# Kernel tuning notes

Measured on AMD Instinct MI355X. Metric: run time of the kernel, lower is better.

The kernel has to match this reference:

```python
import jax, jax.numpy as jnp
import numpy as np

H = 4      # SSM / attn heads (d_model/headdim = 256/64)
WIN = 4    # attention window over bands


def _ln(x, g, b):
    m = jnp.mean(x, -1, keepdims=True)
    v = jnp.mean((x - m) ** 2, -1, keepdims=True)
    return (x - m) * jax.lax.rsqrt(v + 1e-5) * g + b


def setup_inputs() -> dict:
    key = jax.random.key(0)
    ks = jax.random.split(key, 24)
    def rn(i, shape, s=0.05):
        return jax.random.normal(ks[i], shape, jnp.float32) * s
    B, T, K, D = 2, 256, 8, 256
    return {
        "z": rn(0, (B, T, K, D), 1.0),
        "ln1_g": jnp.ones((D,), jnp.float32), "ln1_b": jnp.zeros((D,), jnp.float32),
        "Wx": rn(1, (D, D)), "conv_w": rn(2, (D, 4), 0.3), "Wz": rn(3, (D, D)),
        "Wb": rn(4, (D, H * 128)), "Wc": rn(5, (D, H * 128)), "Wdt": rn(6, (D, H)),
        "dt_bias": rn(7, (H,), 0.5), "A_log": rn(8, (H,), 0.5), "theta": rn(9, (H,), 1.0),
        "D_skip": rn(10, (H,), 1.0), "mimo_U": rn(11, (H, H), 0.5), "mimo_V": rn(12, (H, H), 0.5),
        "Wout": rn(13, (D, D)),
        "ln2_g": jnp.ones((D,), jnp.float32), "ln2_b": jnp.zeros((D,), jnp.float32),
        "attn_in_w": rn(14, (3 * D, D)), "attn_in_b": rn(15, (3 * D,), 0.02),
        "attn_out_w": rn(16, (D, D)), "attn_out_b": jnp.zeros((D,), jnp.float32),
        "ln3_g": jnp.ones((D,), jnp.float32), "ln3_b": jnp.zeros((D,), jnp.float32),
        "Wg": rn(17, (D, 4 * D)), "Wu": rn(18, (D, 4 * D)), "Wd": rn(19, (4 * D, D)),
    }


def _forward(z, ln1_g, ln1_b, Wx, conv_w, Wz, Wb, Wc, Wdt, dt_bias, A_log, theta,
             D_skip, mimo_U, mimo_V, Wout, ln2_g, ln2_b, attn_in_w, attn_in_b,
             attn_out_w, attn_out_b, ln3_g, ln3_b, Wg, Wu, Wd):
    B, T, K, D = z.shape
    P = D // H
    N = Wb.shape[1] // H
    # ---------- (a) intra-band Mamba3 (complex MIMO selective scan) ----------
    u = _ln(z, ln1_g, ln1_b)
    u = jnp.transpose(u, (0, 2, 1, 3)).reshape(B * K, T, D)   # [BK,T,D]
    x = u @ Wx
    # causal depthwise conv1d, kernel 4
    xp = jnp.pad(x, ((0, 0), (3, 0), (0, 0)))
    x = sum(xp[:, k:k + T, :] * conv_w[:, k] for k in range(4))
    x = jax.nn.silu(x)
    xh = x.reshape(B * K, T, H, P)
    Bm = (u @ Wb).reshape(B * K, T, H, N)
    Cm = (u @ Wc).reshape(B * K, T, H, N)
    Mmix = mimo_U @ mimo_V.T                                  # rank-r cross-head coupling
    Bm = jnp.einsum('hg,btgn->bthn', Mmix, Bm)
    dt = jax.nn.softplus(u @ Wdt + dt_bias)                   # [BK,T,H]
    A = -jnp.exp(A_log)                                       # stable real decay
    mag = jnp.exp(dt * A)
    ph = dt * theta                                           # harmonic rotation
    ar, ai = mag * jnp.cos(ph), mag * jnp.sin(ph)
    xs = tuple(jnp.moveaxis(t, 1, 0) for t in (xh, Bm, Cm, dt, ar, ai))
    h0 = jnp.zeros((B * K, H, N, P), x.dtype)

    def step(carry, s):
        h_re, h_im = carry
        xt, bt, ct, dtt, art, ait = s
        dBx = (dtt[:, :, None, None] * bt[:, :, :, None]) * xt[:, :, None, :]
        nr = art[:, :, None, None] * h_re - ait[:, :, None, None] * h_im + dBx
        ni = art[:, :, None, None] * h_im + ait[:, :, None, None] * h_re
        return (nr, ni), jnp.einsum('bhn,bhnp->bhp', ct, nr)   # Re(C . h)

    _, ys = jax.lax.scan(step, (h0, h0), xs)                  # ys: [T,BK,H,P]
    y = jnp.moveaxis(ys, 0, 1) + D_skip[None, None, :, None] * xh
    y = y.reshape(B * K, T, D) * jax.nn.silu(u @ Wz)
    y = y @ Wout
    z = z + jnp.transpose(y.reshape(B, K, T, D), (0, 2, 1, 3))
    # ---------- (b) inter-band windowed attention ----------
    zn = _ln(z, ln2_g, ln2_b).reshape(B * T, K, D)
    qkv = zn @ attn_in_w.T + attn_in_b
    q, k_, v = jnp.split(qkv, 3, axis=-1)
    hd = D // H
    def hs(t):
        return t.reshape(B * T, K // WIN, WIN, H, hd).transpose(0, 1, 3, 2, 4)
    q, k_, v = hs(q), hs(k_), hs(v)
    s = jnp.einsum('mwhqd,mwhkd->mwhqk', q, k_) * jnp.float32(1.0 / np.sqrt(hd))
    a = jax.nn.softmax(s, axis=-1)
    o = jnp.einsum('mwhqk,mwhkd->mwhqd', a, v).transpose(0, 1, 3, 2, 4).reshape(B * T, K, D)
    z = z + (o @ attn_out_w.T + attn_out_b).reshape(B, T, K, D)
    # ---------- (c) SwiGLU FFN ----------
    zf = _ln(z, ln3_g, ln3_b)
    z = z + (jax.nn.silu(zf @ Wg) * (zf @ Wu)) @ Wd
    return z


def reference(z, ln1_g, ln1_b, Wx, conv_w, Wz, Wb, Wc, Wdt, dt_bias, A_log, theta,
              D_skip, mimo_U, mimo_V, Wout, ln2_g, ln2_b, attn_in_w, attn_in_b,
              attn_out_w, attn_out_b, ln3_g, ln3_b, Wg, Wu, Wd):
    return _forward(z, ln1_g, ln1_b, Wx, conv_w, Wz, Wb, Wc, Wdt, dt_bias, A_log,
                    theta, D_skip, mimo_U, mimo_V, Wout, ln2_g, ln2_b, attn_in_w,
                    attn_in_b, attn_out_w, attn_out_b, ln3_g, ln3_b, Wg, Wu, Wd)
```

## Files before the change

### kernel.cpp

```cpp
#include <hip/hip_runtime.h>
#include <hip/hip_bf16.h>
#include <math.h>

typedef __hip_bfloat16 bf16;
typedef __attribute__((ext_vector_type(8))) short s16x8;
typedef __attribute__((ext_vector_type(4))) float f32x4;

__device__ __forceinline__ float siluf(float x) { return x / (1.f + __expf(-x)); }
__device__ __forceinline__ float bits2f(unsigned short u) {
    union { float f; unsigned i; } v; v.i = ((unsigned)u) << 16; return v.f;
}
__device__ __forceinline__ unsigned short f2bits(float f) {
    return (unsigned short)__bfloat16_as_ushort(__float2bfloat16(f));
}

#define KFL 1024
#define OFF_UB   (768*KFL)
#define OFF_DTV  (1280*KFL)
#define OFF_BMB  (1344*KFL)
#define OFF_CMB  (2368*KFL)
#define OFF_ZGB  (3392*KFL)
#define OFF_XB   (3904*KFL)
#define OFF_X2T  (4928*KFL)
#define OFF_P    (5440*KFL)
#define OFF_YGB  (7488*KFL)
#define OFF_Z2   (8000*KFL)
#define OFF_ZFB  (9024*KFL)
#define OFF_GG   OFF_BMB

#define W_BCZX 0
#define W_OUT  393216
#define W_QKV  458752
#define W_AO   655360
#define W_GU   720896
#define W_D    1245184

__global__ __launch_bounds__(256) void prep_ln1_kernel(
    const float* __restrict__ Wx, const float* __restrict__ Wb,
    const float* __restrict__ Wc, const float* __restrict__ Wz,
    const float* __restrict__ Wo, const float* __restrict__ Wqkv,
    const float* __restrict__ Wao, const float* __restrict__ Wg,
    const float* __restrict__ Wu, const float* __restrict__ Wd,
    const float* __restrict__ U, const float* __restrict__ V,
    unsigned short* __restrict__ wout,
    const float* __restrict__ z, const float* __restrict__ g1,
    const float* __restrict__ b1, const float* __restrict__ Wdt,
    const float* __restrict__ dt_bias,
    unsigned short* __restrict__ u, float4* __restrict__ dtv4)
{
    __shared__ __align__(16) float smem[64 * 65];
    int blk = blockIdx.x;
    int tid = threadIdx.x;
    if (blk < 368) {
        if (blk >= 304) {
            int off = blk - 304;
            const float* src; int dst, base;
            if (off < 48) { src = Wqkv; dst = W_QKV; base = off * 4096; }
            else          { src = Wao;  dst = W_AO;  base = (off - 48) * 4096; }
            #pragma unroll
            for (int i = 0; i < 16; i++) {
                int idx = base + tid + i * 256;
                wout[dst + idx] = f2bits(src[idx]);
            }
            return;
        }
        float* lds = smem;
        const float* src; int srcN, n0, sc0, k0, dstoff, dstK, mix = 0, t;
        if (blk < 32)       { t = blk;       src = Wb; srcN = 512;  dstoff = W_BCZX; dstK = 256;
                              n0 = (t >> 2) * 64;        sc0 = 0; k0 = (t & 3) * 64; mix = 1; }
        else if (blk < 64)  { t = blk - 32;  src = Wc; srcN = 512;  dstoff = W_BCZX; dstK = 256;
                              n0 = 512 + (t >> 2) * 64;  sc0 = (t >> 2) * 64; k0 = (t & 3) * 64; }
        else if (blk < 80)  { t = blk - 64;  src = Wz; srcN = 256;  dstoff = W_BCZX; dstK = 256;
                              n0 = 1024 + (t >> 2) * 64; sc0 = (t >> 2) * 64; k0 = (t & 3) * 64; }
        else if (blk < 96)  { t = blk - 80;  src = Wx; srcN = 256;  dstoff = W_BCZX; dstK = 256;
                              n0 = 1280 + (t >> 2) * 64; sc0 = (t >> 2) * 64; k0 = (t & 3) * 64; }
        else if (blk < 112) { t = blk - 96;  src = Wo; srcN = 256;  dstoff = W_OUT;  dstK = 256;
                              n0 = (t >> 2) * 64;        sc0 = n0; k0 = (t & 3) * 64; }
        else if (blk < 176) { t = blk - 112; src = Wg; srcN = 1024; dstoff = W_GU;   dstK = 256;
                              n0 = (t >> 2) * 64;        sc0 = n0; k0 = (t & 3) * 64; }
        else if (blk < 240) { t = blk - 176; src = Wu; srcN = 1024; dstoff = W_GU;   dstK = 256;
                              n0 = 1024 + (t >> 2) * 64; sc0 = (t >> 2) * 64; k0 = (t & 3) * 64; }
        else                { t = blk - 240; src = Wd; srcN = 256;  dstoff = W_D;    dstK = 1024;
                              n0 = (t >> 4) * 64;        sc0 = n0; k0 = (t & 15) * 64; }
        if (mix) {
            int h = n0 >> 7, scol = n0 & 127;
            float mm[4];
            #pragma unroll
            for (int g = 0; g < 4; g++) {
                float s = 0.f;
                #pragma unroll
                for (int j = 0; j < 4; j++) s += U[h * 4 + j] * V[g * 4 + j];
                mm[g] = s;
            }
            #pragma unroll
            for (int i = 0; i < 16; i++) {
                int idx = tid + i * 256;
                int kk = idx >> 6, nn = idx & 63;
                const float* row = src + (size_t)(k0 + kk) * 512 + scol + nn;
                lds[kk * 65 + nn] = mm[0] * row[0] + mm[1] * row[128]
                                  + mm[2] * row[256] + mm[3] * row[384];
            }
        } else {
            #pragma unroll
            for (int i = 0; i < 16; i++) {
                int idx = tid + i * 256;
                int kk = idx >> 6, nn = idx & 63;
                lds[kk * 65 + nn] = src[(size_t)(k0 + kk) * srcN + sc0 + nn];
            }
        }
        __syncthreads();
        #pragma unroll
        for (int i = 0; i < 16; i++) {
            int idx = tid + i * 256;
            int nn = idx >> 6, kk = idx & 63;
            wout[dstoff + (size_t)(n0 + nn) * dstK + k0 + kk] = f2bits(lds[kk * 65 + nn]);
        }
        return;
    }
    int r = blk - 368;
    float* lds = smem;
    float* dts = smem + 4;
    int t = r & 255, bk = r >> 8;
    int b_ = bk >> 3, k = bk & 7;
    int srcr = ((b_ * 256 + t) * 8 + k) * 256;
    int d = tid;
    float x = z[srcr + d];
    float v = x;
    #pragma unroll
    for (int off = 32; off; off >>= 1) v += __shfl_xor(v, off, 64);
    if ((d & 63) == 0) lds[d >> 6] = v;
    __syncthreads();
    float mean = (lds[0] + lds[1] + lds[2] + lds[3]) * (1.f / 256.f);
    __syncthreads();
    float c = x - mean;
    v = c * c;
    #pragma unroll
    for (int off = 32; off; off >>= 1) v += __shfl_xor(v, off, 64);
    if ((d & 63) == 0) lds[d >> 6] = v;
    __syncthreads();
    float var = (lds[0] + lds[1] + lds[2] + lds[3]) * (1.f / 256.f);
    float uval = c * rsqrtf(var + 1e-5f) * g1[d] + b1[d];
    u[r * 256 + d] = f2bits(uval);
    float4 wv = *(const float4*)(Wdt + d * 4);
    float q0 = uval * wv.x, q1 = uval * wv.y, q2 = uval * wv.z, q3 = uval * wv.w;
    #pragma unroll
    for (int off = 32; off; off >>= 1) {
        q0 += __shfl_xor(q0, off, 64);
        q1 += __shfl_xor(q1, off, 64);
        q2 += __shfl_xor(q2, off, 64);
        q3 += __shfl_xor(q3, off, 64);
    }
    if ((d & 63) == 0) {
        int w = d >> 6;
        dts[w * 4 + 0] = q0; dts[w * 4 + 1] = q1;
        dts[w * 4 + 2] = q2; dts[w * 4 + 3] = q3;
    }
    __syncthreads();
    if (d == 0) {
        float dv[4];
        #pragma unroll
        for (int h = 0; h < 4; h++) {
            float xx = dts[h] + dts[4 + h] + dts[8 + h] + dts[12 + h] + dt_bias[h];
            dv[h] = (xx > 20.f) ? xx : log1pf(__expf(xx));
        }
        dtv4[r] = make_float4(dv[0], dv[1], dv[2], dv[3]);
    }
}

__global__ __launch_bounds__(256) void gemm_bczx(
    const unsigned short* __restrict__ A, const unsigned short* __restrict__ Bt,
    unsigned short* __restrict__ bmb, unsigned short* __restrict__ cmb,
    unsigned short* __restrict__ zgb, unsigned short* __restrict__ xb)
{
    __shared__ __align__(16) unsigned short As[64 * 72];
    __shared__ __align__(16) unsigned short Bs[128 * 72];
    const int K = 256;
    int tid = threadIdx.x;
    int n0 = blockIdx.x * 128, m0 = blockIdx.y * 64;
    int w = tid >> 6, l = tid & 63;
    int mwave = (w >> 1) * 32, nwave = (w & 1) * 64;
    f32x4 acc[2][4] = {};
    int srow = tid >> 3, sc = (tid & 7) * 8;
    const unsigned short* Ap = A + (size_t)(m0 + srow) * K + sc;
    const unsigned short* Bp = Bt + (size_t)(n0 + srow) * K + sc;
    int lq = l & 15, lh = l >> 4;
    uint4 a0 = *(const uint4*)(Ap);
    uint4 a1 = *(const uint4*)(Ap + (size_t)32 * K);
    uint4 b0 = *(const uint4*)(Bp);
    uint4 b1 = *(const uint4*)(Bp + (size_t)32 * K);
    uint4 b2 = *(const uint4*)(Bp + (size_t)64 * K);
    uint4 b3 = *(const uint4*)(Bp + (size_t)96 * K);
    for (int k0 = 0; k0 < K; k0 += 64) {
        if (k0) __syncthreads();
        *(uint4*)&As[srow * 72 + sc] = a0;
        *(uint4*)&As[(srow + 32) * 72 + sc] = a1;
        *(uint4*)&Bs[srow * 72 + sc] = b0;
        *(uint4*)&Bs[(srow + 32) * 72 + sc] = b1;
        *(uint4*)&Bs[(srow + 64) * 72 + sc] = b2;
        *(uint4*)&Bs[(srow + 96) * 72 + sc] = b3;
        __syncthreads();
        if (k0 + 64 < K) {
            a0 = *(const uint4*)(Ap + k0 + 64);
            a1 = *(const uint4*)(Ap + (size_t)32 * K + k0 + 64);
            b0 = *(const uint4*)(Bp + k0 + 64);
            b1 = *(const uint4*)(Bp + (size_t)32 * K + k0 + 64);
            b2 = *(const uint4*)(Bp + (size_t)64 * K + k0 + 64);
            b3 = *(const uint4*)(Bp + (size_t)96 * K + k0 + 64);
        }
        #pragma unroll
        for (int kk = 0; kk < 2; kk++) {
            int kof = kk * 32 + lh * 8;
            s16x8 bfr[4];
            #pragma unroll
            for (int nf = 0; nf < 4; nf++)
                bfr[nf] = *(const s16x8*)&Bs[(nwave + nf * 16 + lq) * 72 + kof];
            #pragma unroll
            for (int mf = 0; mf < 2; mf++) {
                s16x8 af = *(const s16x8*)&As[(mwave + mf * 16 + lq) * 72 + kof];
                #pragma unroll
                for (int nf = 0; nf < 4; nf++)
                    acc[mf][nf] = __builtin_amdgcn_mfma_f32_16x16x32_bf16(af, bfr[nf], acc[mf][nf], 0, 0, 0);
            }
        }
    }
    #pragma unroll
    for (int mf = 0; mf < 2; mf++) {
        #pragma unroll
        for (int nf = 0; nf < 4; nf++) {
            int n = n0 + nwave + nf * 16 + lq;
            #pragma unroll
            for (int r = 0; r < 4; r++) {
                int m = m0 + mwave + mf * 16 + lh * 4 + r;
                float v = acc[mf][nf][r];
                if (n < 512)       bmb[(size_t)m * 512 + n] = f2bits(v);
                else if (n < 1024) cmb[(size_t)m * 512 + (n - 512)] = f2bits(v);
                else if (n < 1280) zgb[(size_t)m * 256 + (n - 1024)] = f2bits(siluf(v));
                else               xb[(size_t)m * 256 + (n - 1280)] = f2bits(v);
            }
        }
    }
}

__global__ __launch_bounds__(256) void s_conv_kernel(
    const unsigned short* __restrict__ cmb, const unsigned short* __restrict__ bmb,
    const float4* __restrict__ dtv4, const float* __restrict__ A_log,
    const float* __restrict__ theta, unsigned short* __restrict__ P,
    const unsigned short* __restrict__ xb, const float* __restrict__ cw,
    unsigned short* __restrict__ x2t)
{
    __shared__ __align__(16) char smem[39936];
    int blk = blockIdx.x;
    int tid = threadIdx.x;
    if (blk >= 192) {
        int c = blk - 192;
        int bhid = c >> 2, tt = c & 3;
        int bk = bhid >> 2, h = bhid & 3;
        int t0 = tt * 64;
        float* tile = (float*)smem;
        #pragma unroll
        for (int i = 0; i < 17; i++) {
            int idx = tid + i * 256;
            if (idx < 67 * 64) {
                int tr = idx >> 6, dd = idx & 63;
                int t = t0 - 3 + tr;
                tile[tr * 65 + dd] = (t >= 0)
                    ? bits2f(xb[(size_t)(bk * 256 + t) * 256 + h * 64 + dd]) : 0.f;
            }
        }
        __syncthreads();
        int wv_ = tid >> 6, lt = tid & 63;
        #pragma unroll 4
        for (int pi = 0; pi < 16; pi++) {
            int p = wv_ * 16 + pi;
            float4 wv = *(const float4*)(cw + (h * 64 + p) * 4);
            float acc = tile[lt * 65 + p] * wv.x + tile[(lt + 1) * 65 + p] * wv.y +
                        tile[(lt + 2) * 65 + p] * wv.z + tile[(lt + 3) * 65 + p] * wv.w;
            x2t[(size_t)(bhid * 64 + p) * 256 + t0 + lt] = f2bits(siluf(acc));
        }
        return;
    }
    int map = blk >> 6;
    int bh = blk & 63;
    int bx = (map == 2) ? 1 : 0;
    int by = (map == 0) ? 0 : 1;
    int bk = bh >> 2, h = bh & 3;
    unsigned short* As = (unsigned short*)smem;
    unsigned short* Bs = As + 128 * 72;
    float* mAs = (float*)(smem + 36864);
    float* phs = mAs + 256;
    float* dss = phs + 256;
    int srow = tid >> 3, sc = (tid & 7) * 8;
    const unsigned short* Ap = cmb + (size_t)(bk * 256 + by * 128 + srow) * 512 + h * 128 + sc;
    const unsigned short* Bp = bmb + (size_t)(bk * 256 + bx * 128 + srow) * 512 + h * 128 + sc;
    uint4 a0 = *(const uint4*)(Ap);
    uint4 a1 = *(const uint4*)(Ap + (size_t)32 * 512);
    uint4 a2 = *(const uint4*)(Ap + (size_t)64 * 512);
    uint4 a3 = *(const uint4*)(Ap + (size_t)96 * 512);
    uint4 b0 = *(const uint4*)(Bp);
    uint4 b1 = *(const uint4*)(Bp + (size_t)32 * 512);
    uint4 b2 = *(const uint4*)(Bp + (size_t)64 * 512);
    uint4 b3 = *(const uint4*)(Bp + (size_t)96 * 512);
    {
        float4 dv = dtv4[bk * 256 + tid];
        float dth = (h == 0) ? dv.x : (h == 1) ? dv.y : (h == 2) ? dv.z : dv.w;
        float Ah = -__expf(A_log[h]);
        float th = theta[h];
        float a = dth * Ah, p = dth * th;
        dss[tid] = dth;
        int lane = tid & 63, wv = tid >> 6;
        #pragma unroll
        for (int off = 1; off < 64; off <<= 1) {
            float ta = __shfl_up(a, off, 64);
            float tp = __shfl_up(p, off, 64);
            if (lane >= off) { a += ta; p += tp; }
        }
        if (lane == 63) { mAs[wv] = a; phs[wv] = p; }
        __syncthreads();
        float offA = 0.f, offP = 0.f;
        #pragma unroll
        for (int j = 0; j < 3; j++)
            if (j < wv) { offA += mAs[j]; offP += phs[j]; }
        __syncthreads();
        mAs[tid] = a + offA;
        phs[tid] = p + offP;
        __syncthreads();
    }
    int w = tid >> 6, l = tid & 63;
    int mwave = (w >> 1) * 64, nwave = (w & 1) * 64;
    int lq = l & 15, lh = l >> 4;
    unsigned short* Pout = P + (size_t)bh * 65536;
    f32x4 acc[4][4] = {};
    for (int k0 = 0; k0 < 128; k0 += 64) {
        __syncthreads();
        *(uint4*)&As[srow * 72 + sc] = a0;
        *(uint4*)&As[(srow + 32) * 72 + sc] = a1;
        *(uint4*)&As[(srow + 64) * 72 + sc] = a2;
        *(uint4*)&As[(srow + 96) * 72 + sc] = a3;
        *(uint4*)&Bs[srow * 72 + sc] = b0;
        *(uint4*)&Bs[(srow + 32) * 72 + sc] = b1;
        *(uint4*)&Bs[(srow + 64) * 72 + sc] = b2;
        *(uint4*)&Bs[(srow + 96) * 72 + sc] = b3;
        __syncthreads();
        if (k0 + 64 < 128) {
            a0 = *(const uint4*)(Ap + k0 + 64);
            a1 = *(const uint4*)(Ap + (size_t)32 * 512 + k0 + 64);
            a2 = *(const uint4*)(Ap + (size_t)64 * 512 + k0 + 64);
            a3 = *(const uint4*)(Ap + (size_t)96 * 512 + k0 + 64);
            b0 = *(const uint4*)(Bp + k0 + 64);
            b1 = *(const uint4*)(Bp + (size_t)32 * 512 + k0 + 64);
            b2 = *(const uint4*)(Bp + (size_t)64 * 512 + k0 + 64);
            b3 = *(const uint4*)(Bp + (size_t)96 * 512 + k0 + 64);
        }
        #pragma unroll
        for (int kk = 0; kk < 2; kk++) {
            int kof = kk * 32 + lh * 8;
            s16x8 bfr[4];
            #pragma unroll
            for (int nf = 0; nf < 4; nf++)
                bfr[nf] = *(const s16x8*)&Bs[(nwave + nf * 16 + lq) * 72 + kof];
            #pragma unroll
            for (int mf = 0; mf < 4; mf++) {
                s16x8 af = *(const s16x8*)&As[(mwave + mf * 16 + lq) * 72 + kof];
                #pragma unroll
                for (int nf = 0; nf < 4; nf++)
                    acc[mf][nf] = __builtin_amdgcn_mfma_f32_16x16x32_bf16(af, bfr[nf], acc[mf][nf], 0, 0, 0);
            }
        }
    }
    #pragma unroll
    for (int mf = 0; mf < 4; mf++) {
        float tmv[4], tpv[4]; int tg[4];
        #pragma unroll
        for (int r = 0; r < 4; r++) {
            tg[r] = by * 128 + mwave + mf * 16 + lh * 4 + r;
            tmv[r] = mAs[tg[r]];
            tpv[r] = phs[tg[r]];
        }
        #pragma unroll
        for (int nf = 0; nf < 4; nf++) {
            int s = bx * 128 + nwave + nf * 16 + lq;
            float ms = mAs[s];
            float ps = phs[s];
            float ds = dss[s];
            #pragma unroll
            for (int r = 0; r < 4; r++) {
                float wgt = (s <= tg[r])
                    ? __expf(tmv[r] - ms) * __cosf(tpv[r] - ps) * ds : 0.f;
                Pout[tg[r] * 256 + s] = f2bits(acc[mf][nf][r] * wgt);
            }
        }
    }
}

__global__ __launch_bounds__(256) void gemm_y(
    const unsigned short* __restrict__ P, const unsigned short* __restrict__ x2t,
    const unsigned short* __restrict__ zgb, const float* __restrict__ Dsk,
    unsigned short* __restrict__ ygb)
{
    int by = blockIdx.x, bh = blockIdx.y;
    int bk = bh >> 2, h = bh & 3;
    int t0 = by * 32;
    int tid = threadIdx.x;
    int w = tid >> 6, l = tid & 63;
    int mw = (w >> 1) * 16, nw = (w & 1) * 32;
    int lq = l & 15, lh = l >> 4;
    __shared__ __align__(16) unsigned short As[32 * 72];
    __shared__ __align__(16) unsigned short Bs[64 * 72];
    f32x4 acc[2] = {};
    int srow = tid >> 3, sc = (tid & 7) * 8;
    const unsigned short* Ap = P + (size_t)bh * 65536 + (size_t)(t0 + srow) * 256 + sc;
    const unsigned short* Bp = x2t + (size_t)bh * 16384 + (size_t)srow * 256 + sc;
    int kmax = ((by >> 1) + 1) * 64;
    uint4 a0 = *(const uint4*)(Ap);
    uint4 b0 = *(const uint4*)(Bp);
    uint4 b1 = *(const uint4*)(Bp + (size_t)32 * 256);
    for (int k0 = 0; k0 < kmax; k0 += 64) {
        if (k0) __syncthreads();
        *(uint4*)&As[(srow & 31) * 72 + sc] = a0;
        *(uint4*)&Bs[srow * 72 + sc] = b0;
        *(uint4*)&Bs[(srow + 32) * 72 + sc] = b1;
        __syncthreads();
        if (k0 + 64 < kmax) {
            a0 = *(const uint4*)(Ap + k0 + 64);
            b0 = *(const uint4*)(Bp + k0 + 64);
            b1 = *(const uint4*)(Bp + (size_t)32 * 256 + k0 + 64);
        }
        #pragma unroll
        for (int kk = 0; kk < 2; kk++) {
            int kof = kk * 32 + lh * 8;
            s16x8 af = *(const s16x8*)&As[(mw + lq) * 72 + kof];
            #pragma unroll
            for (int nf = 0; nf < 2; nf++) {
                s16x8 bf = *(const s16x8*)&Bs[(nw + nf * 16 + lq) * 72 + kof];
                acc[nf] = __builtin_amdgcn_mfma_f32_16x16x32_bf16(af, bf, acc[nf], 0, 0, 0);
            }
        }
    }
    float dsk = Dsk[h];
    #pragma unroll
    for (int nf = 0; nf < 2; nf++) {
        int p = nw + nf * 16 + lq;
        #pragma unroll
        for (int r = 0; r < 4; r++) {
            int t = t0 + mw + lh * 4 + r;
            float xv = bits2f(x2t[(size_t)bh * 16384 + p * 256 + t]);
            float zg = bits2f(zgb[(size_t)(bk * 256 + t) * 256 + h * 64 + p]);
            ygb[(size_t)(bk * 256 + t) * 256 + h * 64 + p] =
                f2bits((acc[nf][r] + dsk * xv) * zg);
        }
    }
}

__global__ __launch_bounds__(512) void mid_kernel(
    const unsigned short* __restrict__ ygb, const unsigned short* __restrict__ wts,
    const float* __restrict__ zin,
    const float* __restrict__ g2, const float* __restrict__ b2,
    const float* __restrict__ qbias, const float* __restrict__ obias,
    const float* __restrict__ g3, const float* __restrict__ b3,
    float* __restrict__ z2, unsigned short* __restrict__ zfb)
{
    __shared__ __align__(16) char smem[65024];
    unsigned short* Bs = (unsigned short*)smem;
    unsigned short* As = (unsigned short*)(smem + 36864);
    unsigned short* zn = (unsigned short*)(smem + 39168);
    float* z1s = (float*)(smem + 47616);
    float (*partS)[8] = (float(*)[8])(smem + 64000);
    float (*partQ)[8] = (float(*)[8])(smem + 64512);
    unsigned short* qk = (unsigned short*)smem;

    const int K = 256;
    int tid = threadIdx.x;
    int m0 = blockIdx.x * 16;
    int w = tid >> 6, l = tid & 63;
    int nw = w * 32;
    int lq = l & 15, lh = l >> 4;
    int srow = tid >> 3, sc = (tid & 7) * 8;

    {
        int rb = m0 + (srow & 15);
        int irow = ((rb >> 11) * 8 + (rb & 7)) * 256 + ((rb >> 3) & 255);
        const unsigned short* Ap = ygb + (size_t)irow * K + sc;
        const unsigned short* Bp = wts + W_OUT + (size_t)srow * K + sc;
        f32x4 acc[2] = {};
        uint4 a0 = *(const uint4*)(Ap);
        uint4 c0 = *(const uint4*)(Bp);
        uint4 c1 = *(const uint4*)(Bp + (size_t)64 * K);
        uint4 c2 = *(const uint4*)(Bp + (size_t)128 * K);
        uint4 c3 = *(const uint4*)(Bp + (size_t)192 * K);
        for (int k0 = 0; k0 < K; k0 += 64) {
            if (k0) __syncthreads();
            if (tid < 128) *(uint4*)&As[srow * 72 + sc] = a0;
            *(uint4*)&Bs[srow * 72 + sc] = c0;
            *(uint4*)&Bs[(srow + 64) * 72 + sc] = c1;
            *(uint4*)&Bs[(srow + 128) * 72 + sc] = c2;
            *(uint4*)&Bs[(srow + 192) * 72 + sc] = c3;
            __syncthreads();
            if (k0 + 64 < K) {
                a0 = *(const uint4*)(Ap + k0 + 64);
                c0 = *(const uint4*)(Bp + k0 + 64);
                c1 = *(const uint4*)(Bp + (size_t)64 * K + k0 + 64);
                c2 = *(const uint4*)(Bp + (size_t)128 * K + k0 + 64);
                c3 = *(const uint4*)(Bp + (size_t)192 * K + k0 + 64);
            }
            #pragma unroll
            for (int kk = 0; kk < 2; kk++) {
                int kof = kk * 32 + lh * 8;
                s16x8 af = *(const s16x8*)&As[lq * 72 + kof];
                #pragma unroll
                for (int nf = 0; nf < 2; nf++) {
                    s16x8 bf = *(const s16x8*)&Bs[(nw + nf * 16 + lq) * 72 + kof];
                    acc[nf] = __builtin_amdgcn_mfma_f32_16x16x32_bf16(af, bf, acc[nf], 0, 0, 0);
                }
            }
        }
        #pragma unroll
        for (int r = 0; r < 4; r++) {
            int row = lh * 4 + r;
            float s = 0.f, q = 0.f;
            #pragma unroll
            for (int nf = 0; nf < 2; nf++) {
                float v = acc[nf][r] + zin[(size_t)(m0 + row) * 256 + nw + nf * 16 + lq];
                acc[nf][r] = v;
                s += v; q += v * v;
            }
            #pragma unroll
            for (int off = 1; off < 16; off <<= 1) {
                s += __shfl_xor(s, off, 64);
                q += __shfl_xor(q, off, 64);
            }
            if (lq == 0) { partS[row][w] = s; partQ[row][w] = q; }
        }
        __syncthreads();
        float gv[2], bbv[2];
        #pragma unroll
        for (int nf = 0; nf < 2; nf++) {
            gv[nf] = g2[nw + nf * 16 + lq];
            bbv[nf] = b2[nw + nf * 16 + lq];
        }
        #pragma unroll
        for (int r = 0; r < 4; r++) {
            int row = lh * 4 + r;
            float sum = 0.f, sq = 0.f;
            #pragma unroll
            for (int j = 0; j < 8; j++) { sum += partS[row][j]; sq += partQ[row][j]; }
            float mean = sum * (1.f / 256.f);
            float var = sq * (1.f / 256.f) - mean * mean;
            float rstd = rsqrtf(var + 1e-5f);
            #pragma unroll
            for (int nf = 0; nf < 2; nf++) {
                int n = nw + nf * 16 + lq;
                float v = acc[nf][r];
                z1s[row * 256 + n] = v;
                zn[row * 264 + n] = f2bits((v - mean) * rstd * gv[nf] + bbv[nf]);
            }
        }
    }

    f32x4 aq0[2] = {}, aq1[2] = {}, aq2[2] = {};
#define QKV_PASS(PIDX, AQ) do { \
    const unsigned short* Bp2 = wts + W_QKV + (size_t)((PIDX) * 256 + srow) * 256 + sc; \
    uint4 d0 = *(const uint4*)(Bp2); \
    uint4 d1 = *(const uint4*)(Bp2 + (size_t)64 * 256); \
    uint4 d2 = *(const uint4*)(Bp2 + (size_t)128 * 256); \
    uint4 d3 = *(const uint4*)(Bp2 + (size_t)192 * 256); \
    for (int k0 = 0; k0 < 256; k0 += 64) { \
        __syncthreads(); \
        *(uint4*)&Bs[srow * 72 + sc] = d0; \
        *(uint4*)&Bs[(srow + 64) * 72 + sc] = d1; \
        *(uint4*)&Bs[(srow + 128) * 72 + sc] = d2; \
        *(uint4*)&Bs[(srow + 192) * 72 + sc] = d3; \
        __syncthreads(); \
        if (k0 + 64 < 256) { \
            d0 = *(const uint4*)(Bp2 + k0 + 64); \
            d1 = *(const uint4*)(Bp2 + (size_t)64 * 256 + k0 + 64); \
            d2 = *(const uint4*)(Bp2 + (size_t)128 * 256 + k0 + 64); \
            d3 = *(const uint4*)(Bp2 + (size_t)192 * 256 + k0 + 64); \
        } \
        _Pragma("unroll") \
        for (int kk = 0; kk < 2; kk++) { \
            int kof = kk * 32 + lh * 8; \
            s16x8 af = *(const s16x8*)&zn[lq * 264 + k0 + kof]; \
            _Pragma("unroll") \
            for (int nf = 0; nf < 2; nf++) { \
                s16x8 bf = *(const s16x8*)&Bs[(nw + nf * 16 + lq) * 72 + kof]; \
                AQ[nf] = __builtin_amdgcn_mfma_f32_16x16x32_bf16(af, bf, AQ[nf], 0, 0, 0); \
            } \
        } \
    } \
} while (0)
    QKV_PASS(0, aq0);
    QKV_PASS(1, aq1);
    QKV_PASS(2, aq2);
#undef QKV_PASS

    __syncthreads();
#define QKV_STORE(PIDX, AQ) do { \
    _Pragma("unroll") \
    for (int nf = 0; nf < 2; nf++) { \
        int n = (PIDX) * 256 + nw + nf * 16 + lq; \
        float bb = qbias[n]; \
        _Pragma("unroll") \
        for (int r = 0; r < 4; r++) \
            qk[(lh * 4 + r) * 776 + n] = f2bits(AQ[nf][r] + bb); \
    } \
} while (0)
    QKV_STORE(0, aq0);
    QKV_STORE(1, aq1);
    QKV_STORE(2, aq2);
#undef QKV_STORE
    __syncthreads();
    {
        int hh = w & 3;
        int half = w >> 2;
        int d = l;
        #pragma unroll
        for (int wi = 0; wi < 2; wi++) {
            int w4 = half * 2 + wi;
            int r0 = w4 * 4;
            float qv[4], kv[4], vv[4];
            #pragma unroll
            for (int j = 0; j < 4; j++) {
                qv[j] = bits2f(qk[(r0 + j) * 776 + hh * 64 + d]);
                kv[j] = bits2f(qk[(r0 + j) * 776 + 256 + hh * 64 + d]);
                vv[j] = bits2f(qk[(r0 + j) * 776 + 512 + hh * 64 + d]);
            }
            float sc_[4][4];
            #pragma unroll
            for (int qi = 0; qi < 4; qi++)
                #pragma unroll
                for (int ki = 0; ki < 4; ki++) {
                    float v = qv[qi] * kv[ki];
                    #pragma unroll
                    for (int off = 32; off; off >>= 1) v += __shfl_xor(v, off, 64);
                    sc_[qi][ki] = v * 0.125f;
                }
            #pragma unroll
            for (int qi = 0; qi < 4; qi++) {
                float mx = fmaxf(fmaxf(sc_[qi][0], sc_[qi][1]), fmaxf(sc_[qi][2], sc_[qi][3]));
                float e0 = __expf(sc_[qi][0] - mx), e1 = __expf(sc_[qi][1] - mx);
                float e2 = __expf(sc_[qi][2] - mx), e3 = __expf(sc_[qi][3] - mx);
                float inv = 1.f / (e0 + e1 + e2 + e3);
                float ov = (e0 * vv[0] + e1 * vv[1] + e2 * vv[2] + e3 * vv[3]) * inv;
                zn[(r0 + qi) * 264 + hh * 64 + d] = f2bits(ov);
            }
        }
    }

    {
        f32x4 ac4[2] = {};
        const unsigned short* Bp4 = wts + W_AO + (size_t)srow * K + sc;
        uint4 c0 = *(const uint4*)(Bp4);
        uint4 c1 = *(const uint4*)(Bp4 + (size_t)64 * K);
        uint4 c2 = *(const uint4*)(Bp4 + (size_t)128 * K);
        uint4 c3 = *(const uint4*)(Bp4 + (size_t)192 * K);
        for (int k0 = 0; k0 < K; k0 += 64) {
            __syncthreads();
            *(uint4*)&Bs[srow * 72 + sc] = c0;
            *(uint4*)&Bs[(srow + 64) * 72 + sc] = c1;
            *(uint4*)&Bs[(srow + 128) * 72 + sc] = c2;
            *(uint4*)&Bs[(srow + 192) * 72 + sc] = c3;
            __syncthreads();
            if (k0 + 64 < K) {
                c0 = *(const uint4*)(Bp4 + k0 + 64);
                c1 = *(const uint4*)(Bp4 + (size_t)64 * K + k0 + 64);
                c2 = *(const uint4*)(Bp4 + (size_t)128 * K + k0 + 64);
                c3 = *(const uint4*)(Bp4 + (size_t)192 * K + k0 + 64);
            }
            #pragma unroll
            for (int kk = 0; kk < 2; kk++) {
                int kof = kk * 32 + lh * 8;
                s16x8 af = *(const s16x8*)&zn[lq * 264 + k0 + kof];
                #pragma unroll
                for (int nf = 0; nf < 2; nf++) {
                    s16x8 bf = *(const s16x8*)&Bs[(nw + nf * 16 + lq) * 72 + kof];
                    ac4[nf] = __builtin_amdgcn_mfma_f32_16x16x32_bf16(af, bf, ac4[nf], 0, 0, 0);
                }
            }
        }
        float bv[2], gv[2], bbv[2];
        #pragma unroll
        for (int nf = 0; nf < 2; nf++) {
            int n = nw + nf * 16 + lq;
            bv[nf] = obias[n];
            gv[nf] = g3[n];
            bbv[nf] = b3[n];
        }
        #pragma unroll
        for (int r = 0; r < 4; r++) {
            int row = lh * 4 + r;
            float s = 0.f, q = 0.f;
            #pragma unroll
            for (int nf = 0; nf < 2; nf++) {
                float v = ac4[nf][r] + bv[nf] + z1s[row * 256 + nw + nf * 16 + lq];
                ac4[nf][r] = v;
                s += v; q += v * v;
            }
            #pragma unroll
            for (int off = 1; off < 16; off <<= 1) {
                s += __shfl_xor(s, off, 64);
                q += __shfl_xor(q, off, 64);
            }
            if (lq == 0) { partS[row][w] = s; partQ[row][w] = q; }
        }
        __syncthreads();
        #pragma unroll
        for (int r = 0; r < 4; r++) {
            int row = lh * 4 + r;
            float sum = 0.f, sq = 0.f;
            #pragma unroll
            for (int j = 0; j < 8; j++) { sum += partS[row][j]; sq += partQ[row][j]; }
            float mean = sum * (1.f / 256.f);
            float var = sq * (1.f / 256.f) - mean * mean;
            float rstd = rsqrtf(var + 1e-5f);
            size_t ro = (size_t)(m0 + row) * 256;
            #pragma unroll
            for (int nf = 0; nf < 2; nf++) {
                int n = nw + nf * 16 + lq;
                float v = ac4[nf][r];
                z2[ro + n] = v;
                zfb[ro + n] = f2bits((v - mean) * rstd * gv[nf] + bbv[nf]);
            }
        }
    }
}

__global__ __launch_bounds__(256) void gemm_gu2(
    const unsigned short* __restrict__ A, const unsigned short* __restrict__ Wgu,
    unsigned short* __restrict__ gg)
{
    const int K = 256;
    __shared__ __align__(16) unsigned short As[64 * 72];
    __shared__ __align__(16) unsigned short Bgs[64 * 72];
    __shared__ __align__(16) unsigned short Bus[64 * 72];
    int tid = threadIdx.x;
    int n0 = blockIdx.x * 64, m0 = blockIdx.y * 64;
    int w = tid >> 6, l = tid & 63;
    int mwave = (w >> 1) * 32, nwave = (w & 1) * 32;
    int lq = l & 15, lh = l >> 4;
    f32x4 ag[2][2] = {}, au[2][2] = {};
    int srow = tid >> 3, sc = (tid & 7) * 8;
    const unsigned short* Ap = A + (size_t)(m0 + srow) * K + sc;
    const unsigned short* Bgp = Wgu + (size_t)(n0 + srow) * K + sc;
    const unsigned short* Bup = Wgu + (size_t)(1024 + n0 + srow) * K + sc;
    uint4 a0 = *(const uint4*)(Ap);
    uint4 a1 = *(const uint4*)(Ap + (size_t)32 * K);
    uint4 bg0 = *(const uint4*)(Bgp);
    uint4 bg1 = *(const uint4*)(Bgp + (size_t)32 * K);
    uint4 bu0 = *(const uint4*)(Bup);
    uint4 bu1 = *(const uint4*)(Bup + (size_t)32 * K);
    for (int k0 = 0; k0 < K; k0 += 64) {
        if (k0) __syncthreads();
        *(uint4*)&As[srow * 72 + sc] = a0;
        *(uint4*)&As[(srow + 32) * 72 + sc] = a1;
        *(uint4*)&Bgs[srow * 72 + sc] = bg0;
        *(uint4*)&Bgs[(srow + 32) * 72 + sc] = bg1;
        *(uint4*)&Bus[srow * 72 + sc] = bu0;
        *(uint4*)&Bus[(srow + 32) * 72 + sc] = bu1;
        __syncthreads();
        if (k0 + 64 < K) {
            a0 = *(const uint4*)(Ap + k0 + 64);
            a1 = *(const uint4*)(Ap + (size_t)32 * K + k0 + 64);
            bg0 = *(const uint4*)(Bgp + k0 + 64);
            bg1 = *(const uint4*)(Bgp + (size_t)32 * K + k0 + 64);
            bu0 = *(const uint4*)(Bup + k0 + 64);
            bu1 = *(const uint4*)(Bup + (size_t)32 * K + k0 + 64);
        }
        #pragma unroll
        for (int kk = 0; kk < 2; kk++) {
            int kof = kk * 32 + lh * 8;
            s16x8 bgr[2], bur[2];
            #pragma unroll
            for (int nf = 0; nf < 2; nf++) {
                bgr[nf] = *(const s16x8*)&Bgs[(nwave + nf * 16 + lq) * 72 + kof];
                bur[nf] = *(const s16x8*)&Bus[(nwave + nf * 16 + lq) * 72 + kof];
            }
            #pragma unroll
            for (int mf = 0; mf < 2; mf++) {
                s16x8 af = *(const s16x8*)&As[(mwave + mf * 16 + lq) * 72 + kof];
                #pragma unroll
                for (int nf = 0; nf < 2; nf++) {
                    ag[mf][nf] = __builtin_amdgcn_mfma_f32_16x16x32_bf16(af, bgr[nf], ag[mf][nf], 0, 0, 0);
                    au[mf][nf] = __builtin_amdgcn_mfma_f32_16x16x32_bf16(af, bur[nf], au[mf][nf], 0, 0, 0);
                }
            }
        }
    }
    #pragma unroll
    for (int mf = 0; mf < 2; mf++) {
        #pragma unroll
        for (int nf = 0; nf < 2; nf++) {
            int n = n0 + nwave + nf * 16 + lq;
            #pragma unroll
            for (int r = 0; r < 4; r++) {
                int m = m0 + mwave + mf * 16 + lh * 4 + r;
                gg[(size_t)m * 1024 + n] = f2bits(siluf(ag[mf][nf][r]) * au[mf][nf][r]);
            }
        }
    }
}

__global__ __launch_bounds__(256) void gemm_d2(
    const unsigned short* __restrict__ gg, const unsigned short* __restrict__ Bt,
    const float* __restrict__ resid, float* __restrict__ out)
{
    __shared__ __align__(16) unsigned short As[64 * 72];
    __shared__ __align__(16) unsigned short Bs[32 * 72];
    const int K = 1024, N = 256;
    int tid = threadIdx.x;
    int n0 = blockIdx.x * 32, m0 = blockIdx.y * 64;
    int w = tid >> 6, l = tid & 63;
    int mw = (w >> 1) * 32, nw = (w & 1) * 16;
    f32x4 acc[2] = {};
    int srow = tid >> 3, sc = (tid & 7) * 8;
    const unsigned short* Ap = gg + (size_t)(m0 + srow) * K + sc;
    const unsigned short* Bp = Bt + (size_t)(n0 + (srow & 31)) * K + sc;
    int lq = l & 15, lh = l >> 4;
    uint4 a0 = *(const uint4*)(Ap);
    uint4 a1 = *(const uint4*)(Ap + (size_t)32 * K);
    uint4 b0 = *(const uint4*)(Bp);
    for (int k0 = 0; k0 < K; k0 += 64) {
        if (k0) __syncthreads();
        *(uint4*)&As[srow * 72 + sc] = a0;
        *(uint4*)&As[(srow + 32) * 72 + sc] = a1;
        *(uint4*)&Bs[(srow & 31) * 72 + sc] = b0;
        __syncthreads();
        if (k0 + 64 < K) {
            a0 = *(const uint4*)(Ap + k0 + 64);
            a1 = *(const uint4*)(Ap + (size_t)32 * K + k0 + 64);
            b0 = *(const uint4*)(Bp + k0 + 64);
        }
        #pragma unroll
        for (int kk = 0; kk < 2; kk++) {
            int kof = kk * 32 + lh * 8;
            s16x8 bf = *(const s16x8*)&Bs[(nw + lq) * 72 + kof];
            #pragma unroll
            for (int mf = 0; mf < 2; mf++) {
                s16x8 af = *(const s16x8*)&As[(mw + mf * 16 + lq) * 72 + kof];
                acc[mf] = __builtin_amdgcn_mfma_f32_16x16x32_bf16(af, bf, acc[mf], 0, 0, 0);
            }
        }
    }
    int n = n0 + nw + lq;
    #pragma unroll
    for (int mf = 0; mf < 2; mf++) {
        #pragma unroll
        for (int r = 0; r < 4; r++) {
            int m = m0 + mw + mf * 16 + lh * 4 + r;
            out[(size_t)m * N + n] = acc[mf][r] + resid[(size_t)m * N + n];
        }
    }
}

extern "C" void kernel_launch(void* const* d_in, const int* in_sizes, int n_in,
                              void* d_out, int out_size, void* d_ws, size_t ws_size,
                              hipStream_t stream)
{
    const float* z         = (const float*)d_in[0];
    const float* ln1_g     = (const float*)d_in[1];
    const float* ln1_b     = (const float*)d_in[2];
    const float* Wx        = (const float*)d_in[3];
    const float* conv_w    = (const float*)d_in[4];
    const float* Wz        = (const float*)d_in[5];
    const float* Wb        = (const float*)d_in[6];
    const float* Wc        = (const float*)d_in[7];
    const float* Wdt       = (const float*)d_in[8];
    const float* dt_bias   = (const float*)d_in[9];
    const float* A_log     = (const float*)d_in[10];
    const float* theta     = (const float*)d_in[11];
    const float* D_skip    = (const float*)d_in[12];
    const float* mimo_U    = (const float*)d_in[13];
    const float* mimo_V    = (const float*)d_in[14];
    const float* Wout      = (const float*)d_in[15];
    const float* ln2_g     = (const float*)d_in[16];
    const float* ln2_b     = (const float*)d_in[17];
    const float* attn_in_w = (const float*)d_in[18];
    const float* attn_in_b = (const float*)d_in[19];
    const float* attn_out_w= (const float*)d_in[20];
    const float* attn_out_b= (const float*)d_in[21];
    const float* ln3_g     = (const float*)d_in[22];
    const float* ln3_b     = (const float*)d_in[23];
    const float* Wg        = (const float*)d_in[24];
    const float* Wu        = (const float*)d_in[25];
    const float* Wd        = (const float*)d_in[26];

    float* W = (float*)d_ws;
    unsigned short* wts = (unsigned short*)W;
    unsigned short* ub  = (unsigned short*)(W + OFF_UB);
    float4* dtv4        = (float4*)(W + OFF_DTV);
    unsigned short* bmb = (unsigned short*)(W + OFF_BMB);
    unsigned short* cmb = (unsigned short*)(W + OFF_CMB);
    unsigned short* zgb = (unsigned short*)(W + OFF_ZGB);
    unsigned short* xb  = (unsigned short*)(W + OFF_XB);
    unsigned short* x2t = (unsigned short*)(W + OFF_X2T);
    unsigned short* pbuf= (unsigned short*)(W + OFF_P);
    unsigned short* ygb = (unsigned short*)(W + OFF_YGB);
    float* z2           = W + OFF_Z2;
    unsigned short* zfb = (unsigned short*)(W + OFF_ZFB);
    unsigned short* gg  = (unsigned short*)(W + OFF_GG);

    prep_ln1_kernel<<<4464, 256, 0, stream>>>(
        Wx, Wb, Wc, Wz, Wout, attn_in_w, attn_out_w, Wg, Wu, Wd, mimo_U, mimo_V,
        wts, z, ln1_g, ln1_b, Wdt, dt_bias, ub, dtv4);
    gemm_bczx<<<dim3(12, 64), 256, 0, stream>>>(ub, wts + W_BCZX, bmb, cmb, zgb, xb);
    s_conv_kernel<<<448, 256, 0, stream>>>(cmb, bmb, dtv4, A_log, theta, pbuf,
                                           xb, conv_w, x2t);
    gemm_y<<<dim3(8, 64), 256, 0, stream>>>(pbuf, x2t, zgb, D_skip, ygb);
    mid_kernel<<<256, 512, 0, stream>>>(ygb, wts, z, ln2_g, ln2_b,
                                        attn_in_b, attn_out_b, ln3_g, ln3_b,
                                        z2, zfb);
    gemm_gu2<<<dim3(16, 64), 256, 0, stream>>>(zfb, wts + W_GU, gg);
    gemm_d2<<<dim3(8, 64), 256, 0, stream>>>(gg, wts + W_D, z2, (float*)d_out);
}
```

Measured before the change: 192.8 us.

## Deepen register prefetch to two stages across chained GEMMs in fused attention kernel

Replaces the per-GEMM one-stage register prefetch in the fused out-proj/LN/QKV/attn-out kernel with a continuous two-buffer pipeline. Weight tiles for the next GEMM (QKV passes, then attn-out) start loading while the current one is still computing, which removes the pipeline bubbles at GEMM boundaries. The down-projection GEMM is likewise changed to keep two K-tiles in flight in registers. The cost is higher register pressure, which may lower occupancy or cause spills.

```diff
diff --git a/kernel.cpp b/kernel.cpp
--- a/kernel.cpp
+++ b/kernel.cpp
@@ -476,51 +476,95 @@
     int lq = l & 15, lh = l >> 4;
     int srow = tid >> 3, sc = (tid & 7) * 8;
 
+    const unsigned short* BpO  = wts + W_OUT + (size_t)srow * K + sc;
+    const unsigned short* BpQ0 = wts + W_QKV + (size_t)srow * K + sc;
+    const unsigned short* BpQ1 = BpQ0 + (size_t)256 * K;
+    const unsigned short* BpQ2 = BpQ0 + (size_t)512 * K;
+    const unsigned short* BpA  = wts + W_AO + (size_t)srow * K + sc;
+
+    uint4 wA0, wA1, wA2, wA3, wB0, wB1, wB2, wB3;
+
+#define LOADW(P, BASE, KO) do { \
+    P##0 = *(const uint4*)((BASE) + (KO)); \
+    P##1 = *(const uint4*)((BASE) + (size_t)64 * K + (KO)); \
+    P##2 = *(const uint4*)((BASE) + (size_t)128 * K + (KO)); \
+    P##3 = *(const uint4*)((BASE) + (size_t)192 * K + (KO)); \
+} while (0)
+#define STORE_BS(P) do { \
+    *(uint4*)&Bs[srow * 72 + sc] = P##0; \
+    *(uint4*)&Bs[(srow + 64) * 72 + sc] = P##1; \
+    *(uint4*)&Bs[(srow + 128) * 72 + sc] = P##2; \
+    *(uint4*)&Bs[(srow + 192) * 72 + sc] = P##3; \
+} while (0)
+#define MM_ZN(AQ, KO) do { \
+    _Pragma("unroll") \
+    for (int kk = 0; kk < 2; kk++) { \
+        int kof = kk * 32 + lh * 8; \
+        s16x8 af = *(const s16x8*)&zn[lq * 264 + (KO) + kof]; \
+        _Pragma("unroll") \
+        for (int nf = 0; nf < 2; nf++) { \
+            s16x8 bf = *(const s16x8*)&Bs[(nw + nf * 16 + lq) * 72 + kof]; \
+            AQ[nf] = __builtin_amdgcn_mfma_f32_16x16x32_bf16(af, bf, AQ[nf], 0, 0, 0); \
+        } \
+    } \
+} while (0)
+#define MM_AS(AQ) do { \
+    _Pragma("unroll") \
+    for (int kk = 0; kk < 2; kk++) { \
+        int kof = kk * 32 + lh * 8; \
+        s16x8 af = *(const s16x8*)&As[lq * 72 + kof]; \
+        _Pragma("unroll") \
+        for (int nf = 0; nf < 2; nf++) { \
+            s16x8 bf = *(const s16x8*)&Bs[(nw + nf * 16 + lq) * 72 + kof]; \
+            AQ[nf] = __builtin_amdgcn_mfma_f32_16x16x32_bf16(af, bf, AQ[nf], 0, 0, 0); \
+        } \
+    } \
+} while (0)
+
+    f32x4 acc1[2] = {};
     {
         int rb = m0 + (srow & 15);
         int irow = ((rb >> 11) * 8 + (rb & 7)) * 256 + ((rb >> 3) & 255);
         const unsigned short* Ap = ygb + (size_t)irow * K + sc;
-        const unsigned short* Bp = wts + W_OUT + (size_t)srow * K + sc;
-        f32x4 acc[2] = {};
-        uint4 a0 = *(const uint4*)(Ap);
-        uint4 c0 = *(const uint4*)(Bp);
-        uint4 c1 = *(const uint4*)(Bp + (size_t)64 * K);
-        uint4 c2 = *(const uint4*)(Bp + (size_t)128 * K);
-        uint4 c3 = *(const uint4*)(Bp + (size_t)192 * K);
-        for (int k0 = 0; k0 < K; k0 += 64) {
-            if (k0) __syncthreads();
-            if (tid < 128) *(uint4*)&As[srow * 72 + sc] = a0;
-            *(uint4*)&Bs[srow * 72 + sc] = c0;
-            *(uint4*)&Bs[(srow + 64) * 72 + sc] = c1;
-            *(uint4*)&Bs[(srow + 128) * 72 + sc] = c2;
-            *(uint4*)&Bs[(srow + 192) * 72 + sc] = c3;
-            __syncthreads();
-            if (k0 + 64 < K) {
-                a0 = *(const uint4*)(Ap + k0 + 64);
-                c0 = *(const uint4*)(Bp + k0 + 64);
-                c1 = *(const uint4*)(Bp + (size_t)64 * K + k0 + 64);
-                c2 = *(const uint4*)(Bp + (size_t)128 * K + k0 + 64);
-                c3 = *(const uint4*)(Bp + (size_t)192 * K + k0 + 64);
-            }
-            #pragma unroll
-            for (int kk = 0; kk < 2; kk++) {
-                int kof = kk * 32 + lh * 8;
-                s16x8 af = *(const s16x8*)&As[lq * 72 + kof];
-                #pragma unroll
-                for (int nf = 0; nf < 2; nf++) {
-                    s16x8 bf = *(const s16x8*)&Bs[(nw + nf * 16 + lq) * 72 + kof];
-                    acc[nf] = __builtin_amdgcn_mfma_f32_16x16x32_bf16(af, bf, acc[nf], 0, 0, 0);
-                }
-            }
-        }
+        LOADW(wA, BpO, 0);
+        LOADW(wB, BpO, 64);
+        uint4 aP = *(const uint4*)(Ap);
+        uint4 aQ;
+        __syncthreads();
+        if (tid < 128) *(uint4*)&As[srow * 72 + sc] = aP;
+        STORE_BS(wA);
+        __syncthreads();
+        aQ = *(const uint4*)(Ap + 64);
+        LOADW(wA, BpO, 128);
+        MM_AS(acc1);
+        __syncthreads();
+        if (tid < 128) *(uint4*)&As[srow * 72 + sc] = aQ;
+        STORE_BS(wB);
+        __syncthreads();
+        aP = *(const uint4*)(Ap + 128);
+        LOADW(wB, BpO, 192);
+        MM_AS(acc1);
+        __syncthreads();
+        if (tid < 128) *(uint4*)&As[srow * 72 + sc] = aP;
+        STORE_BS(wA);
+        __syncthreads();
+        aQ = *(const uint4*)(Ap + 192);
+        LOADW(wA, BpQ0, 0);
+        MM_AS(acc1);
+        __syncthreads();
+        if (tid < 128) *(uint4*)&As[srow * 72 + sc] = aQ;
+        STORE_BS(wB);
+        __syncthreads();
+        LOADW(wB, BpQ0, 64);
+        MM_AS(acc1);
         #pragma unroll
         for (int r = 0; r < 4; r++) {
             int row = lh * 4 + r;
             float s = 0.f, q = 0.f;
             #pragma unroll
             for (int nf = 0; nf < 2; nf++) {
-                float v = acc[nf][r] + zin[(size_t)(m0 + row) * 256 + nw + nf * 16 + lq];
-                acc[nf][r] = v;
+                float v = acc1[nf][r] + zin[(size_t)(m0 + row) * 256 + nw + nf * 16 + lq];
+                acc1[nf][r] = v;
                 s += v; q += v * v;
             }
             #pragma unroll
@@ -549,7 +593,7 @@
             #pragma unroll
             for (int nf = 0; nf < 2; nf++) {
                 int n = nw + nf * 16 + lq;
-                float v = acc[nf][r];
+                float v = acc1[nf][r];
                 z1s[row * 256 + n] = v;
                 zn[row * 264 + n] = f2bits((v - mean) * rstd * gv[nf] + bbv[nf]);
             }
@@ -557,41 +601,31 @@
     }
 
     f32x4 aq0[2] = {}, aq1[2] = {}, aq2[2] = {};
-#define QKV_PASS(PIDX, AQ) do { \
-    const unsigned short* Bp2 = wts + W_QKV + (size_t)((PIDX) * 256 + srow) * 256 + sc; \
-    uint4 d0 = *(const uint4*)(Bp2); \
-    uint4 d1 = *(const uint4*)(Bp2 + (size_t)64 * 256); \
-    uint4 d2 = *(const uint4*)(Bp2 + (size_t)128 * 256); \
-    uint4 d3 = *(const uint4*)(Bp2 + (size_t)192 * 256); \
-    for (int k0 = 0; k0 < 256; k0 += 64) { \
-        __syncthreads(); \
-        *(uint4*)&Bs[srow * 72 + sc] = d0; \
-        *(uint4*)&Bs[(srow + 64) * 72 + sc] = d1; \
-        *(uint4*)&Bs[(srow + 128) * 72 + sc] = d2; \
-        *(uint4*)&Bs[(srow + 192) * 72 + sc] = d3; \
-        __syncthreads(); \
-        if (k0 + 64 < 256) { \
-            d0 = *(const uint4*)(Bp2 + k0 + 64); \
-            d1 = *(const uint4*)(Bp2 + (size_t)64 * 256 + k0 + 64); \
-            d2 = *(const uint4*)(Bp2 + (size_t)128 * 256 + k0 + 64); \
-            d3 = *(const uint4*)(Bp2 + (size_t)192 * 256 + k0 + 64); \
-        } \
-        _Pragma("unroll") \
-        for (int kk = 0; kk < 2; kk++) { \
-            int kof = kk * 32 + lh * 8; \
-            s16x8 af = *(const s16x8*)&zn[lq * 264 + k0 + kof]; \
-            _Pragma("unroll") \
-            for (int nf = 0; nf < 2; nf++) { \
-                s16x8 bf = *(const s16x8*)&Bs[(nw + nf * 16 + lq) * 72 + kof]; \
-                AQ[nf] = __builtin_amdgcn_mfma_f32_16x16x32_bf16(af, bf, AQ[nf], 0, 0, 0); \
-            } \
-        } \
-    } \
+#define RND(P, AQ, KO, NBASE, NKO) do { \
+    __syncthreads(); \
+    STORE_BS(P); \
+    __syncthreads(); \
+    LOADW(P, NBASE, NKO); \
+    MM_ZN(AQ, KO); \
 } while (0)
-    QKV_PASS(0, aq0);
-    QKV_PASS(1, aq1);
-    QKV_PASS(2, aq2);
-#undef QKV_PASS
+#define RND_NL(P, AQ, KO) do { \
+    __syncthreads(); \
+    STORE_BS(P); \
+    __syncthreads(); \
+    MM_ZN(AQ, KO); \
+} while (0)
+    RND(wA, aq0, 0,   BpQ0, 128);
+    RND(wB, aq0, 64,  BpQ0, 192);
+    RND(wA, aq0, 128, BpQ1, 0);
+    RND(wB, aq0, 192, BpQ1, 64);
+    RND(wA, aq1, 0,   BpQ1, 128);
+    RND(wB, aq1, 64,  BpQ1, 192);
+    RND(wA, aq1, 128, BpQ2, 0);
+    RND(wB, aq1, 192, BpQ2, 64);
+    RND(wA, aq2, 0,   BpQ2, 128);
+    RND(wB, aq2, 64,  BpQ2, 192);
+    RND(wA, aq2, 128, BpA, 0);
+    RND(wB, aq2, 192, BpA, 64);
 
     __syncthreads();
 #define QKV_STORE(PIDX, AQ) do { \
@@ -648,35 +682,10 @@
 
     {
         f32x4 ac4[2] = {};
-        const unsigned short* Bp4 = wts + W_AO + (size_t)srow * K + sc;
-        uint4 c0 = *(const uint4*)(Bp4);
-        uint4 c1 = *(const uint4*)(Bp4 + (size_t)64 * K);
-        uint4 c2 = *(const uint4*)(Bp4 + (size_t)128 * K);
-        uint4 c3 = *(const uint4*)(Bp4 + (size_t)192 * K);
-        for (int k0 = 0; k0 < K; k0 += 64) {
-            __syncthreads();
-            *(uint4*)&Bs[srow * 72 + sc] = c0;
-            *(uint4*)&Bs[(srow + 64) * 72 + sc] = c1;
-            *(uint4*)&Bs[(srow + 128) * 72 + sc] = c2;
-            *(uint4*)&Bs[(srow + 192) * 72 + sc] = c3;
-            __syncthreads();
-            if (k0 + 64 < K) {
-                c0 = *(const uint4*)(Bp4 + k0 + 64);
-                c1 = *(const uint4*)(Bp4 + (size_t)64 * K + k0 + 64);
-                c2 = *(const uint4*)(Bp4 + (size_t)128 * K + k0 + 64);
-                c3 = *(const uint4*)(Bp4 + (size_t)192 * K + k0 + 64);
-            }
-            #pragma unroll
-            for (int kk = 0; kk < 2; kk++) {
-                int kof = kk * 32 + lh * 8;
-                s16x8 af = *(const s16x8*)&zn[lq * 264 + k0 + kof];
-                #pragma unroll
-                for (int nf = 0; nf < 2; nf++) {
-                    s16x8 bf = *(const s16x8*)&Bs[(nw + nf * 16 + lq) * 72 + kof];
-                    ac4[nf] = __builtin_amdgcn_mfma_f32_16x16x32_bf16(af, bf, ac4[nf], 0, 0, 0);
-                }
-            }
-        }
+        RND(wA, ac4, 0,  BpA, 128);
+        RND(wB, ac4, 64, BpA, 192);
+        RND_NL(wA, ac4, 128);
+        RND_NL(wB, ac4, 192);
         float bv[2], gv[2], bbv[2];
         #pragma unroll
         for (int nf = 0; nf < 2; nf++) {
@@ -722,6 +731,12 @@
             }
         }
     }
+#undef RND
+#undef RND_NL
+#undef LOADW
+#undef STORE_BS
+#undef MM_ZN
+#undef MM_AS
 }
 
 __global__ __launch_bounds__(256) void gemm_gu2(
@@ -815,19 +830,42 @@
     const unsigned short* Ap = gg + (size_t)(m0 + srow) * K + sc;
     const unsigned short* Bp = Bt + (size_t)(n0 + (srow & 31)) * K + sc;
     int lq = l & 15, lh = l >> 4;
-    uint4 a0 = *(const uint4*)(Ap);
-    uint4 a1 = *(const uint4*)(Ap + (size_t)32 * K);
-    uint4 b0 = *(const uint4*)(Bp);
-    for (int k0 = 0; k0 < K; k0 += 64) {
-        if (k0) __syncthreads();
-        *(uint4*)&As[srow * 72 + sc] = a0;
-        *(uint4*)&As[(srow + 32) * 72 + sc] = a1;
-        *(uint4*)&Bs[(srow & 31) * 72 + sc] = b0;
-        __syncthreads();
-        if (k0 + 64 < K) {
-            a0 = *(const uint4*)(Ap + k0 + 64);
-            a1 = *(const uint4*)(Ap + (size_t)32 * K + k0 + 64);
-            b0 = *(const uint4*)(Bp + k0 + 64);
+    uint4 xA0 = *(const uint4*)(Ap);
+    uint4 xA1 = *(const uint4*)(Ap + (size_t)32 * K);
+    uint4 yA  = *(const uint4*)(Bp);
+    uint4 xB0 = *(const uint4*)(Ap + 64);
+    uint4 xB1 = *(const uint4*)(Ap + (size_t)32 * K + 64);
+    uint4 yB  = *(const uint4*)(Bp + 64);
+    for (int k0 = 0; k0 < K; k0 += 128) {
+        __syncthreads();
+        *(uint4*)&As[srow * 72 + sc] = xA0;
+        *(uint4*)&As[(srow + 32) * 72 + sc] = xA1;
+        *(uint4*)&Bs[(srow & 31) * 72 + sc] = yA;
+        __syncthreads();
+        if (k0 + 128 < K) {
+            xA0 = *(const uint4*)(Ap + k0 + 128);
+            xA1 = *(const uint4*)(Ap + (size_t)32 * K + k0 + 128);
+            yA  = *(const uint4*)(Bp + k0 + 128);
+        }
+        #pragma unroll
+        for (int kk = 0; kk < 2; kk++) {
+            int kof = kk * 32 + lh * 8;
+            s16x8 bf = *(const s16x8*)&Bs[(nw + lq) * 72 + kof];
+            #pragma unroll
+            for (int mf = 0; mf < 2; mf++) {
+                s16x8 af = *(const s16x8*)&As[(mw + mf * 16 + lq) * 72 + kof];
+                acc[mf] = __builtin_amdgcn_mfma_f32_16x16x32_bf16(af, bf, acc[mf], 0, 0, 0);
+            }
+        }
+        __syncthreads();
+        *(uint4*)&As[srow * 72 + sc] = xB0;
+        *(uint4*)&As[(srow + 32) * 72 + sc] = xB1;
+        *(uint4*)&Bs[(srow & 31) * 72 + sc] = yB;
+        __syncthreads();
+        if (k0 + 192 < K) {
+            xB0 = *(const uint4*)(Ap + k0 + 192);
+            xB1 = *(const uint4*)(Ap + (size_t)32 * K + k0 + 192);
+            yB  = *(const uint4*)(Bp + k0 + 192);
         }
         #pragma unroll
         for (int kk = 0; kk < 2; kk++) {
```

Measured after the change: 190.5 us, median of 2. Within noise of the previous version (-1.2%).
